# Optimization experiments

Measured on AMD Instinct MI355X. Metric: run time of the kernel, lower is better.

## Reference

```python
import jax, jax.numpy as jnp
import numpy as np

B, N, K, C, CE, H = 2, 2048, 48, 128, 128, 128
IN = 2 * C + CE  # 384
AGG_SCALE = 30.0
LN_EPS = 1e-5


def setup_inputs() -> dict:
    key = jax.random.key(0)
    ks = jax.random.split(key, 12)
    inp = {
        "node_h": jax.random.normal(ks[0], (B, N, C), jnp.float32),
        "edge_h": jax.random.normal(ks[1], (B, N, K, CE), jnp.float32),
        "edge_index": jax.random.randint(ks[2], (B, N, K), 0, N, jnp.int64),
        # message MLP: Linear(IN,H) GELU Linear(H,H) GELU Linear(H,C)
        "W1": jax.random.normal(ks[3], (IN, H), jnp.float32) / np.sqrt(IN),
        "b1": jnp.zeros((H,), jnp.float32),
        "W2": jax.random.normal(ks[4], (H, H), jnp.float32) / np.sqrt(H),
        "b2": jnp.zeros((H,), jnp.float32),
        "W3": jax.random.normal(ks[5], (H, C), jnp.float32) / np.sqrt(H),
        "b3": jnp.zeros((C,), jnp.float32),
        "Wu": jax.random.normal(ks[6], (C, C), jnp.float32) / np.sqrt(C),
        "bu": jnp.zeros((C,), jnp.float32),
        "ln_g": jnp.ones((C,), jnp.float32),
        "ln_b": jnp.zeros((C,), jnp.float32),
    }
    return inp


def _layer_norm(x, g, b):
    mu = jnp.mean(x, axis=-1, keepdims=True)
    var = jnp.var(x, axis=-1, keepdims=True)
    return (x - mu) * jax.lax.rsqrt(var + LN_EPS) * g + b


def _gelu(x):
    return jax.nn.gelu(x, approximate=False)  # torch nn.GELU default (erf)


def reference(node_h, edge_h, edge_index, W1, b1, W2, b2, W3, b3, Wu, bu, ln_g, ln_b):
    b, n, k = edge_index.shape
    c = node_h.shape[-1]
    # gather neighbor node features: (B,N,K,C)
    node_j = jnp.take_along_axis(
        node_h, edge_index.reshape(b, n * k)[..., None], axis=1
    ).reshape(b, n, k, c)
    node_i = jnp.broadcast_to(node_h[:, :, None, :], (b, n, k, c))
    edge_packed = jnp.concatenate([node_i, node_j, edge_h], axis=-1)  # (B,N,K,IN)
    # message MLP
    h = _gelu(edge_packed @ W1 + b1)
    h = _gelu(h @ W2 + b2)
    messages = (h @ W3 + b3).sum(axis=-2) / AGG_SCALE  # (B,N,C)
    # dropout is identity in eval mode
    updated_nodes = _layer_norm(node_h + messages, ln_g, ln_b)
    node_updates = updated_nodes @ Wu + bu
    out = _layer_norm(node_h + node_updates, ln_g, ln_b)
    return out
```

## Files before the change

kernel.cpp:

```cpp
#include <hip/hip_runtime.h>
#include <hip/hip_bf16.h>
#include <math.h>

#define Bn   2
#define Nn   2048
#define Kn   48
#define Cn   128
#define G2   16

typedef short bf16x8 __attribute__((ext_vector_type(8)));
typedef float f32x4  __attribute__((ext_vector_type(4)));

#if __has_builtin(__builtin_amdgcn_cvt_pk_bf16_f32)
#define HAS_PK 1
#endif

__device__ __forceinline__ short f2bf(float f) {
  union { float f; unsigned u; } v; v.f = f;
  unsigned r = v.u + 0x7fffu + ((v.u >> 16) & 1u);
  return (short)(r >> 16);
}

__device__ __forceinline__ unsigned pk2(float a, float b) {
#ifdef HAS_PK
  auto p = __builtin_amdgcn_cvt_pk_bf16_f32(a, b);
  return __builtin_bit_cast(unsigned, p);
#else
  return (unsigned)(unsigned short)f2bf(a) | ((unsigned)(unsigned short)f2bf(b) << 16);
#endif
}

__device__ __forceinline__ float gelu_f(float x) {
  float z = x * (-2.3021991f - 0.10294200f * x * x);
  float e = __builtin_amdgcn_exp2f(z);
  return x * __builtin_amdgcn_rcpf(1.0f + e);
}

#define LBAR()                                              \
  do {                                                      \
    __builtin_amdgcn_sched_barrier(0);                      \
    asm volatile("s_waitcnt lgkmcnt(0)" ::: "memory");      \
    __builtin_amdgcn_s_barrier();                           \
    __builtin_amdgcn_sched_barrier(0);                      \
  } while (0)

__global__ void pack_weights(const float* __restrict__ W1,
                             const float* __restrict__ W2,
                             const float* __restrict__ W3,
                             const float* __restrict__ Wu,
                             short* __restrict__ ws) {
  int tid = blockIdx.x * blockDim.x + threadIdx.x;
  if (tid >= 192 * 64) return;
  int lane = tid & 63;
  int tile = tid >> 6;
  const float* W; short* dst;
  if (tile < 32)       { W = W1;         dst = ws; }
  else if (tile < 96)  { W = W1 + 16384; dst = ws + 16384; tile -= 32; }
  else if (tile < 128) { W = W2;         dst = ws + 49152; tile -= 96; }
  else if (tile < 160) { W = W3;         dst = ws + 65536; tile -= 128; }
  else                 { W = Wu;         dst = ws + 81920; tile -= 160; }
  int kt = tile >> 3, nt = tile & 7;
  int n  = nt * 16 + (lane & 15);
  int k0 = kt * 32 + (lane >> 4) * 8;
  union { short s[8]; bf16x8 v; } u8;
#pragma unroll
  for (int j = 0; j < 8; j++) u8.s[j] = f2bf(W[(k0 + j) * 128 + n]);
  *reinterpret_cast<bf16x8*>(dst + (tile << 9) + lane * 8) = u8.v;
}

__global__ __launch_bounds__(512, 4)
void node_update_kernel(const float* __restrict__ node_h,
                        const float* __restrict__ edge_h,
                        const int*   __restrict__ edge_index,
                        const short* __restrict__ wpack,
                        const float* __restrict__ b1,
                        const float* __restrict__ b2,
                        float* __restrict__ hs_out) {
  __shared__ __align__(16) char smem[49664];
  short* Xs  = (short*)smem;
  short* H1s = (short*)smem;
  short* Es  = (short*)(smem + 24576);
  short* nhb = (short*)(smem + 49152);

  const int tid  = threadIdx.x;
  const int n0   = blockIdx.x * 2;
  const int bb   = n0 >> 11;
  const int lane = tid & 63;
  const int wave = tid >> 6;
  const int wn   = wave & 3;
  const int wm   = wave >> 2;
  const int lr   = lane & 15;
  const int lq   = lane >> 4;
  const int gw   = tid & 15;
  const int gr   = tid >> 4;

  const short* W1i = wpack;
  const short* W1e = wpack + 16384;
  const short* W2p = wpack + 49152;

  bf16x8 w1i0[4], w1i1[4];
#pragma unroll
  for (int kt = 0; kt < 4; kt++) {
    w1i0[kt] = *reinterpret_cast<const bf16x8*>(W1i + ((kt * 8 + 2 * wn)     << 9) + lane * 8);
    w1i1[kt] = *reinterpret_cast<const bf16x8*>(W1i + ((kt * 8 + 2 * wn + 1) << 9) + lane * 8);
  }
  const int col0 = wn * 32 + lr;
  const int col1 = col0 + 16;
  const float b1v0 = b1[col0], b1v1 = b1[col1];
  const float b2v0 = b2[col0], b2v1 = b2[col1];
  int idxr[3];
#pragma unroll
  for (int k = 0; k < 3; k++)
    idxr[k] = edge_index[n0 * Kn + gr + k * 32];
  if (tid < 256) nhb[tid] = f2bf(node_h[(size_t)n0 * Cn + tid]);
  LBAR();

  float4 na[3], nb[3];
#pragma unroll
  for (int k = 0; k < 3; k++) {
    const float* src = node_h + ((size_t)(bb * Nn) + idxr[k]) * Cn + gw * 8;
    na[k] = *reinterpret_cast<const float4*>(src);
    nb[k] = *reinterpret_cast<const float4*>(src + 4);
  }
  __builtin_amdgcn_sched_barrier(0);

  float4 ea[3], eb[3];
#pragma unroll
  for (int k = 0; k < 3; k++) {
    int r = gr + k * 32;
    const float* src = edge_h + ((size_t)n0 * Kn + r) * Cn + gw * 8;
    ea[k] = *reinterpret_cast<const float4*>(src);
    eb[k] = *reinterpret_cast<const float4*>(src + 4);
  }
  __builtin_amdgcn_sched_barrier(0);

  f32x4 accY0 = {}, accY1 = {};
#pragma unroll
  for (int kt = 0; kt < 4; kt++) {
    bf16x8 av = {};
    if (lr == 0)
      av = *reinterpret_cast<const bf16x8*>(&nhb[wm * 128 + kt * 32 + lq * 8]);
    accY0 = __builtin_amdgcn_mfma_f32_16x16x32_bf16(av, w1i0[kt], accY0, 0, 0, 0);
    accY1 = __builtin_amdgcn_mfma_f32_16x16x32_bf16(av, w1i1[kt], accY1, 0, 0, 0);
  }
  const float yi0 = __shfl(accY0[0], lr) + b1v0;
  const float yi1 = __shfl(accY1[0], lr) + b1v1;

#pragma unroll
  for (int k = 0; k < 3; k++) {
    int r = gr + k * 32;
    uint4 p;
    p.x = pk2(na[k].x, na[k].y); p.y = pk2(na[k].z, na[k].w);
    p.z = pk2(nb[k].x, nb[k].y); p.w = pk2(nb[k].z, nb[k].w);
    *reinterpret_cast<uint4*>(&Xs[r * 128 + ((gw ^ (r & 7)) << 3)]) = p;
  }
  LBAR();

  f32x4 acc[3][2] = {};
#pragma unroll
  for (int kt = 0; kt < 4; kt++) {
    bf16x8 bf0 = *reinterpret_cast<const bf16x8*>(W1e + ((kt * 8 + 2 * wn)     << 9) + lane * 8);
    bf16x8 bf1 = *reinterpret_cast<const bf16x8*>(W1e + ((kt * 8 + 2 * wn + 1) << 9) + lane * 8);
    int sw = (((kt * 4 + lq) ^ (lr & 7)) << 3);
#pragma unroll
    for (int mt = 0; mt < 3; mt++) {
      bf16x8 a = *reinterpret_cast<const bf16x8*>(&Xs[(wm * 48 + mt * 16 + lr) * 128 + sw]);
      acc[mt][0] = __builtin_amdgcn_mfma_f32_16x16x32_bf16(a, bf0, acc[mt][0], 0, 0, 0);
      acc[mt][1] = __builtin_amdgcn_mfma_f32_16x16x32_bf16(a, bf1, acc[mt][1], 0, 0, 0);
    }
  }

#pragma unroll
  for (int k = 0; k < 3; k++) {
    int r = gr + k * 32;
    uint4 p;
    p.x = pk2(ea[k].x, ea[k].y); p.y = pk2(ea[k].z, ea[k].w);
    p.z = pk2(eb[k].x, eb[k].y); p.w = pk2(eb[k].z, eb[k].w);
    *reinterpret_cast<uint4*>(&Es[r * 128 + ((gw ^ (r & 7)) << 3)]) = p;
  }
  LBAR();

#pragma unroll
  for (int kt = 0; kt < 4; kt++) {
    bf16x8 bf0 = *reinterpret_cast<const bf16x8*>(W1e + (((kt + 4) * 8 + 2 * wn)     << 9) + lane * 8);
    bf16x8 bf1 = *reinterpret_cast<const bf16x8*>(W1e + (((kt + 4) * 8 + 2 * wn + 1) << 9) + lane * 8);
    int sw = (((kt * 4 + lq) ^ (lr & 7)) << 3);
#pragma unroll
    for (int mt = 0; mt < 3; mt++) {
      bf16x8 a = *reinterpret_cast<const bf16x8*>(&Es[(wm * 48 + mt * 16 + lr) * 128 + sw]);
      acc[mt][0] = __builtin_amdgcn_mfma_f32_16x16x32_bf16(a, bf0, acc[mt][0], 0, 0, 0);
      acc[mt][1] = __builtin_amdgcn_mfma_f32_16x16x32_bf16(a, bf1, acc[mt][1], 0, 0, 0);
    }
  }

  {
    const int g0 = col0 >> 3, cl0 = col0 & 7;
    const int g1 = col1 >> 3, cl1 = col1 & 7;
#pragma unroll
    for (int mt = 0; mt < 3; mt++) {
      int r0 = wm * 48 + mt * 16 + lq * 4;
      {
        float v0 = gelu_f(acc[mt][0][0] + yi0);
        float v1 = gelu_f(acc[mt][0][1] + yi0);
        float v2 = gelu_f(acc[mt][0][2] + yi0);
        float v3 = gelu_f(acc[mt][0][3] + yi0);
        unsigned p01 = pk2(v0, v1), p23 = pk2(v2, v3);
        H1s[(r0 + 0) * 128 + ((g0 ^ ((r0 + 0) & 7)) << 3) + cl0] = (short)(p01 & 0xffff);
        H1s[(r0 + 1) * 128 + ((g0 ^ ((r0 + 1) & 7)) << 3) + cl0] = (short)(p01 >> 16);
        H1s[(r0 + 2) * 128 + ((g0 ^ ((r0 + 2) & 7)) << 3) + cl0] = (short)(p23 & 0xffff);
        H1s[(r0 + 3) * 128 + ((g0 ^ ((r0 + 3) & 7)) << 3) + cl0] = (short)(p23 >> 16);
      }
      {
        float v0 = gelu_f(acc[mt][1][0] + yi1);
        float v1 = gelu_f(acc[mt][1][1] + yi1);
        float v2 = gelu_f(acc[mt][1][2] + yi1);
        float v3 = gelu_f(acc[mt][1][3] + yi1);
        unsigned p01 = pk2(v0, v1), p23 = pk2(v2, v3);
        H1s[(r0 + 0) * 128 + ((g1 ^ ((r0 + 0) & 7)) << 3) + cl1] = (short)(p01 & 0xffff);
        H1s[(r0 + 1) * 128 + ((g1 ^ ((r0 + 1) & 7)) << 3) + cl1] = (short)(p01 >> 16);
        H1s[(r0 + 2) * 128 + ((g1 ^ ((r0 + 2) & 7)) << 3) + cl1] = (short)(p23 & 0xffff);
        H1s[(r0 + 3) * 128 + ((g1 ^ ((r0 + 3) & 7)) << 3) + cl1] = (short)(p23 >> 16);
      }
    }
  }
  LBAR();

  f32x4 acc2[3][2] = {};
#pragma unroll
  for (int kt = 0; kt < 4; kt++) {
    bf16x8 bf0 = *reinterpret_cast<const bf16x8*>(W2p + ((kt * 8 + 2 * wn)     << 9) + lane * 8);
    bf16x8 bf1 = *reinterpret_cast<const bf16x8*>(W2p + ((kt * 8 + 2 * wn + 1) << 9) + lane * 8);
    int sw = (((kt * 4 + lq) ^ (lr & 7)) << 3);
#pragma unroll
    for (int mt = 0; mt < 3; mt++) {
      bf16x8 a = *reinterpret_cast<const bf16x8*>(&H1s[(wm * 48 + mt * 16 + lr) * 128 + sw]);
      acc2[mt][0] = __builtin_amdgcn_mfma_f32_16x16x32_bf16(a, bf0, acc2[mt][0], 0, 0, 0);
      acc2[mt][1] = __builtin_amdgcn_mfma_f32_16x16x32_bf16(a, bf1, acc2[mt][1], 0, 0, 0);
    }
  }
  {
    float s0 = 0.f, s1 = 0.f;
#pragma unroll
    for (int mt = 0; mt < 3; mt++)
#pragma unroll
      for (int r = 0; r < 4; r++) {
        s0 += gelu_f(acc2[mt][0][r] + b2v0);
        s1 += gelu_f(acc2[mt][1][r] + b2v1);
      }
    s0 += __shfl_xor(s0, 16);
    s0 += __shfl_xor(s0, 32);
    s1 += __shfl_xor(s1, 16);
    s1 += __shfl_xor(s1, 32);
    if (lq == 0) {
      hs_out[(size_t)(n0 + wm) * Cn + col0] = s0;
      hs_out[(size_t)(n0 + wm) * Cn + col1] = s1;
    }
  }
}

__global__ __launch_bounds__(256, 4)
void tail_kernel(const float* __restrict__ node_h,
                 const short* __restrict__ wpack,
                 const float* __restrict__ b3,
                 const float* __restrict__ bu,
                 const float* __restrict__ ln_g,
                 const float* __restrict__ ln_b,
                 float* __restrict__ out) {
  __shared__ __align__(16) char sm2[24832];
  short* hsB = (short*)sm2;
  float* nhr = (float*)(sm2 + 4096);
  float* xs  = (float*)(sm2 + 12288);
  short* usB = (short*)(sm2 + 20736);

  const int tid  = threadIdx.x;
  const int lane = tid & 63;
  const int wave = tid >> 6;
  const int lr   = lane & 15;
  const int lq   = lane >> 4;
  const int n0   = blockIdx.x * G2;

  const short* W3p = wpack + 65536;
  const short* Wup = wpack + 81920;

  {
    int row = tid >> 4, seg = tid & 15;
    const float* p = node_h + (size_t)(n0 + row) * Cn + seg * 8;
    float4 a0 = *reinterpret_cast<const float4*>(p);
    float4 a1 = *reinterpret_cast<const float4*>(p + 4);
    *reinterpret_cast<float4*>(&nhr[row * 128 + seg * 8])     = a0;
    *reinterpret_cast<float4*>(&nhr[row * 128 + seg * 8 + 4]) = a1;
    const float* q = out + (size_t)(n0 + row) * Cn + seg * 8;
    float4 c0 = *reinterpret_cast<const float4*>(q);
    float4 c1 = *reinterpret_cast<const float4*>(q + 4);
    uint4 pk;
    pk.x = pk2(c0.x, c0.y); pk.y = pk2(c0.z, c0.w);
    pk.z = pk2(c1.x, c1.y); pk.w = pk2(c1.z, c1.w);
    *reinterpret_cast<uint4*>(&hsB[row * 128 + ((seg ^ (row & 7)) << 3)]) = pk;
  }
  __syncthreads();

  f32x4 am[2] = {};
#pragma unroll
  for (int kt = 0; kt < 4; kt++) {
    bf16x8 av = *reinterpret_cast<const bf16x8*>(&hsB[lr * 128 + (((kt * 4 + lq) ^ (lr & 7)) << 3)]);
    bf16x8 bv0 = *reinterpret_cast<const bf16x8*>(W3p + ((kt * 8 + wave * 2 + 0) << 9) + lane * 8);
    bf16x8 bv1 = *reinterpret_cast<const bf16x8*>(W3p + ((kt * 8 + wave * 2 + 1) << 9) + lane * 8);
    am[0] = __builtin_amdgcn_mfma_f32_16x16x32_bf16(av, bv0, am[0], 0, 0, 0);
    am[1] = __builtin_amdgcn_mfma_f32_16x16x32_bf16(av, bv1, am[1], 0, 0, 0);
  }
#pragma unroll
  for (int j = 0; j < 2; j++) {
    int col = (wave * 2 + j) * 16 + lr;
    float bb = 48.0f * b3[col];
#pragma unroll
    for (int r = 0; r < 4; r++) {
      int row = lq * 4 + r;
      xs[row * 132 + col] = nhr[row * 128 + col] + (am[j][r] + bb) * (1.0f / 30.0f);
    }
  }
  __syncthreads();

  const float lg1 = ln_g[lane],      lb1v = ln_b[lane];
  const float lg2 = ln_g[lane + 64], lb2v = ln_b[lane + 64];
#pragma unroll
  for (int s = 0; s < 4; s++) {
    int row = wave * 4 + s;
    float v1 = xs[row * 132 + lane];
    float v2 = xs[row * 132 + lane + 64];
    float s1 = v1 + v2, s2 = v1 * v1 + v2 * v2;
#pragma unroll
    for (int off = 32; off >= 1; off >>= 1) {
      s1 += __shfl_xor(s1, off);
      s2 += __shfl_xor(s2, off);
    }
    float mu = s1 * (1.f / 128.f);
    float var = s2 * (1.f / 128.f) - mu * mu;
    float rstd = rsqrtf(var + 1e-5f);
    unsigned u12 = pk2((v1 - mu) * rstd * lg1 + lb1v,
                       (v2 - mu) * rstd * lg2 + lb2v);
    int sw = (row & 7);
    usB[row * 128 + (((lane >> 3) ^ sw) << 3) + (lane & 7)]       = (short)(u12 & 0xffff);
    usB[row * 128 + ((((lane >> 3) + 8) ^ sw) << 3) + (lane & 7)] = (short)(u12 >> 16);
  }
  __syncthreads();

  f32x4 au[2] = {};
#pragma unroll
  for (int kt = 0; kt < 4; kt++) {
    bf16x8 av = *reinterpret_cast<const bf16x8*>(&usB[lr * 128 + (((kt * 4 + lq) ^ (lr & 7)) << 3)]);
    bf16x8 bv0 = *reinterpret_cast<const bf16x8*>(Wup + ((kt * 8 + wave * 2 + 0) << 9) + lane * 8);
    bf16x8 bv1 = *reinterpret_cast<const bf16x8*>(Wup + ((kt * 8 + wave * 2 + 1) << 9) + lane * 8);
    au[0] = __builtin_amdgcn_mfma_f32_16x16x32_bf16(av, bv0, au[0], 0, 0, 0);
    au[1] = __builtin_amdgcn_mfma_f32_16x16x32_bf16(av, bv1, au[1], 0, 0, 0);
  }
  __syncthreads();
#pragma unroll
  for (int j = 0; j < 2; j++) {
    int col = (wave * 2 + j) * 16 + lr;
    float bb = bu[col];
#pragma unroll
    for (int r = 0; r < 4; r++) {
      int row = lq * 4 + r;
      xs[row * 132 + col] = nhr[row * 128 + col] + au[j][r] + bb;
    }
  }
  __syncthreads();

#pragma unroll
  for (int s = 0; s < 4; s++) {
    int row = wave * 4 + s;
    float v1 = xs[row * 132 + lane];
    float v2 = xs[row * 132 + lane + 64];
    float s1 = v1 + v2, s2 = v1 * v1 + v2 * v2;
#pragma unroll
    for (int off = 32; off >= 1; off >>= 1) {
      s1 += __shfl_xor(s1, off);
      s2 += __shfl_xor(s2, off);
    }
    float mu = s1 * (1.f / 128.f);
    float var = s2 * (1.f / 128.f) - mu * mu;
    float rstd = rsqrtf(var + 1e-5f);
    out[(size_t)(n0 + row) * Cn + lane]      = (v1 - mu) * rstd * lg1 + lb1v;
    out[(size_t)(n0 + row) * Cn + lane + 64] = (v2 - mu) * rstd * lg2 + lb2v;
  }
}

extern "C" void kernel_launch(void* const* d_in, const int* in_sizes, int n_in,
                              void* d_out, int out_size, void* d_ws, size_t ws_size,
                              hipStream_t stream) {
  const float* node_h     = (const float*)d_in[0];
  const float* edge_h     = (const float*)d_in[1];
  const int*   edge_index = (const int*)  d_in[2];
  const float* W1 = (const float*)d_in[3];
  const float* b1 = (const float*)d_in[4];
  const float* W2 = (const float*)d_in[5];
  const float* b2 = (const float*)d_in[6];
  const float* W3 = (const float*)d_in[7];
  const float* b3 = (const float*)d_in[8];
  const float* Wu = (const float*)d_in[9];
  const float* bu = (const float*)d_in[10];
  const float* ln_g = (const float*)d_in[11];
  const float* ln_b = (const float*)d_in[12];
  float* out   = (float*)d_out;
  short* wpack = (short*)d_ws;

  pack_weights<<<48, 256, 0, stream>>>(W1, W2, W3, Wu, wpack);
  node_update_kernel<<<(Bn * Nn) / 2, 512, 0, stream>>>(
      node_h, edge_h, edge_index, wpack, b1, b2, out);
  tail_kernel<<<(Bn * Nn) / G2, 256, 0, stream>>>(
      node_h, wpack, b3, bu, ln_g, ln_b, out);
}
```

Before: 200.7 us.

## Precompute per-node W1 neighbor projection and gather projected rows instead of raw features

A new zprep kernel computes node_h @ W1_j once per node in bf16 and stores it in the output buffer used as scratch. The main kernel gathers these projected rows for neighbors instead of raw node features. It then adds them into the accumulator through an identity-matrix MFMA, which removes the per-edge neighbor GEMM (a third of the first-layer K dimension). It also drops the preloaded W1i registers and writes the aggregated hidden sums as bf16 into the scratch. This adds an extra launch and another bf16 rounding of the projected activations.

```diff
diff --git a/kernel.cpp b/kernel.cpp
--- a/kernel.cpp
+++ b/kernel.cpp
@@ -43,6 +43,7 @@
     __builtin_amdgcn_s_barrier();                           \
     __builtin_amdgcn_sched_barrier(0);                      \
   } while (0)
+
 
 __global__ void pack_weights(const float* __restrict__ W1,
                              const float* __restrict__ W2,
@@ -69,17 +70,64 @@
 }
 
 __global__ __launch_bounds__(512, 4)
+void zprep_kernel(const float* __restrict__ node_h,
+                  const short* __restrict__ wpack,
+                  short* __restrict__ out_s) {
+  __shared__ __align__(16) short Xsp[64 * 128];
+  const int tid  = threadIdx.x;
+  const int n0   = blockIdx.x * 64;
+  const int lane = tid & 63;
+  const int wave = tid >> 6;
+  const int lr   = lane & 15;
+  const int lq   = lane >> 4;
+
+#pragma unroll
+  for (int s = 0; s < 2; s++) {
+    int slot = tid + s * 512;
+    int row = slot >> 4, g = slot & 15;
+    const float* src = node_h + (size_t)(n0 + row) * Cn + g * 8;
+    float4 v0 = *reinterpret_cast<const float4*>(src);
+    float4 v1 = *reinterpret_cast<const float4*>(src + 4);
+    uint4 p;
+    p.x = pk2(v0.x, v0.y); p.y = pk2(v0.z, v0.w);
+    p.z = pk2(v1.x, v1.y); p.w = pk2(v1.z, v1.w);
+    *reinterpret_cast<uint4*>(&Xsp[row * 128 + ((g ^ (row & 7)) << 3)]) = p;
+  }
+  __syncthreads();
+
+  const short* W1e = wpack + 16384;
+  f32x4 acc[4] = {};
+#pragma unroll
+  for (int kt = 0; kt < 4; kt++) {
+    bf16x8 bf = *reinterpret_cast<const bf16x8*>(W1e + ((kt * 8 + wave) << 9) + lane * 8);
+    int sw = (((kt * 4 + lq) ^ (lr & 7)) << 3);
+#pragma unroll
+    for (int mt = 0; mt < 4; mt++) {
+      bf16x8 a = *reinterpret_cast<const bf16x8*>(&Xsp[(mt * 16 + lr) * 128 + sw]);
+      acc[mt] = __builtin_amdgcn_mfma_f32_16x16x32_bf16(a, bf, acc[mt], 0, 0, 0);
+    }
+  }
+  const int col = wave * 16 + lr;
+#pragma unroll
+  for (int mt = 0; mt < 4; mt++)
+#pragma unroll
+    for (int r = 0; r < 4; r++) {
+      int row = n0 + mt * 16 + lq * 4 + r;
+      out_s[(size_t)row * 256 + 128 + col] = f2bf(acc[mt][r]);
+    }
+}
+
+__global__ __launch_bounds__(512, 4)
 void node_update_kernel(const float* __restrict__ node_h,
                         const float* __restrict__ edge_h,
                         const int*   __restrict__ edge_index,
                         const short* __restrict__ wpack,
                         const float* __restrict__ b1,
                         const float* __restrict__ b2,
-                        float* __restrict__ hs_out) {
+                        short* __restrict__ out_s) {
   __shared__ __align__(16) char smem[49664];
   short* Xs  = (short*)smem;
   short* H1s = (short*)smem;
-  short* Es  = (short*)(smem + 24576);
   short* nhb = (short*)(smem + 49152);
 
   const int tid  = threadIdx.x;
@@ -98,30 +146,30 @@
   const short* W1e = wpack + 16384;
   const short* W2p = wpack + 49152;
 
-  bf16x8 w1i0[4], w1i1[4];
-#pragma unroll
-  for (int kt = 0; kt < 4; kt++) {
-    w1i0[kt] = *reinterpret_cast<const bf16x8*>(W1i + ((kt * 8 + 2 * wn)     << 9) + lane * 8);
-    w1i1[kt] = *reinterpret_cast<const bf16x8*>(W1i + ((kt * 8 + 2 * wn + 1) << 9) + lane * 8);
-  }
-  const int col0 = wn * 32 + lr;
-  const int col1 = col0 + 16;
-  const float b1v0 = b1[col0], b1v1 = b1[col1];
-  const float b2v0 = b2[col0], b2v1 = b2[col1];
   int idxr[3];
 #pragma unroll
   for (int k = 0; k < 3; k++)
     idxr[k] = edge_index[n0 * Kn + gr + k * 32];
   if (tid < 256) nhb[tid] = f2bf(node_h[(size_t)n0 * Cn + tid]);
+
+  const int col0 = wn * 32 + lr, col1 = col0 + 16;
+  const float b1v0 = b1[col0], b1v1 = b1[col1];
+  const float b2v0 = b2[col0], b2v1 = b2[col1];
+
+  union { short s[8]; bf16x8 v; } u0 = {}, u1 = {};
+  {
+    int k0 = lq * 8;
+    if (lr - k0 >= 0 && lr - k0 < 8)           u0.s[lr - k0] = (short)0x3F80;
+    if (lr + 16 - k0 >= 0 && lr + 16 - k0 < 8) u1.s[lr + 16 - k0] = (short)0x3F80;
+  }
+  const bf16x8 id0 = u0.v, id1 = u1.v;
   LBAR();
 
-  float4 na[3], nb[3];
-#pragma unroll
-  for (int k = 0; k < 3; k++) {
-    const float* src = node_h + ((size_t)(bb * Nn) + idxr[k]) * Cn + gw * 8;
-    na[k] = *reinterpret_cast<const float4*>(src);
-    nb[k] = *reinterpret_cast<const float4*>(src + 4);
-  }
+  uint4 zj[3];
+#pragma unroll
+  for (int k = 0; k < 3; k++)
+    zj[k] = *reinterpret_cast<const uint4*>(
+        out_s + ((size_t)(bb * Nn) + idxr[k]) * 256 + 128 + gw * 8);
   __builtin_amdgcn_sched_barrier(0);
 
   float4 ea[3], eb[3];
@@ -140,8 +188,10 @@
     bf16x8 av = {};
     if (lr == 0)
       av = *reinterpret_cast<const bf16x8*>(&nhb[wm * 128 + kt * 32 + lq * 8]);
-    accY0 = __builtin_amdgcn_mfma_f32_16x16x32_bf16(av, w1i0[kt], accY0, 0, 0, 0);
-    accY1 = __builtin_amdgcn_mfma_f32_16x16x32_bf16(av, w1i1[kt], accY1, 0, 0, 0);
+    bf16x8 bv0 = *reinterpret_cast<const bf16x8*>(W1i + ((kt * 8 + 2 * wn)     << 9) + lane * 8);
+    bf16x8 bv1 = *reinterpret_cast<const bf16x8*>(W1i + ((kt * 8 + 2 * wn + 1) << 9) + lane * 8);
+    accY0 = __builtin_amdgcn_mfma_f32_16x16x32_bf16(av, bv0, accY0, 0, 0, 0);
+    accY1 = __builtin_amdgcn_mfma_f32_16x16x32_bf16(av, bv1, accY1, 0, 0, 0);
   }
   const float yi0 = __shfl(accY0[0], lr) + b1v0;
   const float yi1 = __shfl(accY1[0], lr) + b1v1;
@@ -149,37 +199,19 @@
 #pragma unroll
   for (int k = 0; k < 3; k++) {
     int r = gr + k * 32;
-    uint4 p;
-    p.x = pk2(na[k].x, na[k].y); p.y = pk2(na[k].z, na[k].w);
-    p.z = pk2(nb[k].x, nb[k].y); p.w = pk2(nb[k].z, nb[k].w);
-    *reinterpret_cast<uint4*>(&Xs[r * 128 + ((gw ^ (r & 7)) << 3)]) = p;
-  }
-  LBAR();
-
-  f32x4 acc[3][2] = {};
-#pragma unroll
-  for (int kt = 0; kt < 4; kt++) {
-    bf16x8 bf0 = *reinterpret_cast<const bf16x8*>(W1e + ((kt * 8 + 2 * wn)     << 9) + lane * 8);
-    bf16x8 bf1 = *reinterpret_cast<const bf16x8*>(W1e + ((kt * 8 + 2 * wn + 1) << 9) + lane * 8);
-    int sw = (((kt * 4 + lq) ^ (lr & 7)) << 3);
-#pragma unroll
-    for (int mt = 0; mt < 3; mt++) {
-      bf16x8 a = *reinterpret_cast<const bf16x8*>(&Xs[(wm * 48 + mt * 16 + lr) * 128 + sw]);
-      acc[mt][0] = __builtin_amdgcn_mfma_f32_16x16x32_bf16(a, bf0, acc[mt][0], 0, 0, 0);
-      acc[mt][1] = __builtin_amdgcn_mfma_f32_16x16x32_bf16(a, bf1, acc[mt][1], 0, 0, 0);
-    }
-  }
-
+    *reinterpret_cast<uint4*>(&Xs[r * 256 + ((16 + (gw ^ (r & 7))) << 3)]) = zj[k];
+  }
 #pragma unroll
   for (int k = 0; k < 3; k++) {
     int r = gr + k * 32;
     uint4 p;
     p.x = pk2(ea[k].x, ea[k].y); p.y = pk2(ea[k].z, ea[k].w);
     p.z = pk2(eb[k].x, eb[k].y); p.w = pk2(eb[k].z, eb[k].w);
-    *reinterpret_cast<uint4*>(&Es[r * 128 + ((gw ^ (r & 7)) << 3)]) = p;
+    *reinterpret_cast<uint4*>(&Xs[r * 256 + ((gw ^ (r & 7)) << 3)]) = p;
   }
   LBAR();
 
+  f32x4 acc[3][2] = {};
 #pragma unroll
   for (int kt = 0; kt < 4; kt++) {
     bf16x8 bf0 = *reinterpret_cast<const bf16x8*>(W1e + (((kt + 4) * 8 + 2 * wn)     << 9) + lane * 8);
@@ -187,11 +219,21 @@
     int sw = (((kt * 4 + lq) ^ (lr & 7)) << 3);
 #pragma unroll
     for (int mt = 0; mt < 3; mt++) {
-      bf16x8 a = *reinterpret_cast<const bf16x8*>(&Es[(wm * 48 + mt * 16 + lr) * 128 + sw]);
+      bf16x8 a = *reinterpret_cast<const bf16x8*>(&Xs[(wm * 48 + mt * 16 + lr) * 256 + sw]);
       acc[mt][0] = __builtin_amdgcn_mfma_f32_16x16x32_bf16(a, bf0, acc[mt][0], 0, 0, 0);
       acc[mt][1] = __builtin_amdgcn_mfma_f32_16x16x32_bf16(a, bf1, acc[mt][1], 0, 0, 0);
     }
   }
+  {
+#pragma unroll
+    for (int mt = 0; mt < 3; mt++) {
+      int swz = ((16 + ((wn * 4 + lq) ^ (lr & 7))) << 3);
+      bf16x8 az = *reinterpret_cast<const bf16x8*>(&Xs[(wm * 48 + mt * 16 + lr) * 256 + swz]);
+      acc[mt][0] = __builtin_amdgcn_mfma_f32_16x16x32_bf16(az, id0, acc[mt][0], 0, 0, 0);
+      acc[mt][1] = __builtin_amdgcn_mfma_f32_16x16x32_bf16(az, id1, acc[mt][1], 0, 0, 0);
+    }
+  }
+  LBAR();
 
   {
     const int g0 = col0 >> 3, cl0 = col0 & 7;
@@ -252,8 +294,8 @@
     s1 += __shfl_xor(s1, 16);
     s1 += __shfl_xor(s1, 32);
     if (lq == 0) {
-      hs_out[(size_t)(n0 + wm) * Cn + col0] = s0;
-      hs_out[(size_t)(n0 + wm) * Cn + col1] = s1;
+      out_s[(size_t)(n0 + wm) * 256 + col0] = f2bf(s0);
+      out_s[(size_t)(n0 + wm) * 256 + col1] = f2bf(s1);
     }
   }
 }
@@ -281,6 +323,7 @@
 
   const short* W3p = wpack + 65536;
   const short* Wup = wpack + 81920;
+  const short* out_s = (const short*)out;
 
   {
     int row = tid >> 4, seg = tid & 15;
@@ -289,13 +332,9 @@
     float4 a1 = *reinterpret_cast<const float4*>(p + 4);
     *reinterpret_cast<float4*>(&nhr[row * 128 + seg * 8])     = a0;
     *reinterpret_cast<float4*>(&nhr[row * 128 + seg * 8 + 4]) = a1;
-    const float* q = out + (size_t)(n0 + row) * Cn + seg * 8;
-    float4 c0 = *reinterpret_cast<const float4*>(q);
-    float4 c1 = *reinterpret_cast<const float4*>(q + 4);
-    uint4 pk;
-    pk.x = pk2(c0.x, c0.y); pk.y = pk2(c0.z, c0.w);
-    pk.z = pk2(c1.x, c1.y); pk.w = pk2(c1.z, c1.w);
-    *reinterpret_cast<uint4*>(&hsB[row * 128 + ((seg ^ (row & 7)) << 3)]) = pk;
+    uint4 h = *reinterpret_cast<const uint4*>(
+        out_s + (size_t)(n0 + row) * 256 + seg * 8);
+    *reinterpret_cast<uint4*>(&hsB[row * 128 + ((seg ^ (row & 7)) << 3)]) = h;
   }
   __syncthreads();
 
@@ -402,11 +441,13 @@
   const float* ln_g = (const float*)d_in[11];
   const float* ln_b = (const float*)d_in[12];
   float* out   = (float*)d_out;
+  short* out_s = (short*)d_out;
   short* wpack = (short*)d_ws;
 
   pack_weights<<<48, 256, 0, stream>>>(W1, W2, W3, Wu, wpack);
+  zprep_kernel<<<(Bn * Nn) / 64, 512, 0, stream>>>(node_h, wpack, out_s);
   node_update_kernel<<<(Bn * Nn) / 2, 512, 0, stream>>>(
-      node_h, edge_h, edge_index, wpack, b1, b2, out);
+      node_h, edge_h, edge_index, wpack, b1, b2, out_s);
   tail_kernel<<<(Bn * Nn) / G2, 256, 0, stream>>>(
       node_h, wpack, b3, bu, ln_g, ln_b, out);
 }
```

After: 206.7 us. 1.03x slower.
